# Optimization experiments

Hardware: AMD Instinct MI355X
Metric: run time of the kernel (lower is better)

The kernel has to match this reference:

```python
import jax, jax.numpy as jnp
import numpy as np

NUM_VARS = 50
EDGE_TYPES = 4
N_HID = 256
MSG_HID = N_HID // 8  # 32
IN_SIZE = 16
BATCH = 512
SKIP_FIRST = True

_adj = np.ones((NUM_VARS, NUM_VARS)) - np.eye(NUM_VARS)
SEND_EDGES, RECV_EDGES = np.where(_adj)
NUM_EDGES = SEND_EDGES.shape[0]  # 2450


def _lin(key, fan_in, fan_out):
    k1, k2 = jax.random.split(key)
    bound = 1.0 / np.sqrt(fan_in)
    w = jax.random.uniform(k1, (fan_in, fan_out), jnp.float32, -bound, bound)
    b = jax.random.uniform(k2, (fan_out,), jnp.float32, -bound, bound)
    return w, b


def setup_inputs() -> dict:
    key = jax.random.key(0)
    ks = jax.random.split(key, 10)
    inputs = jax.random.normal(ks[0], (BATCH, NUM_VARS, IN_SIZE), jnp.float32)
    edges = jax.random.uniform(ks[1], (BATCH, NUM_EDGES, EDGE_TYPES), jnp.float32)
    # per-edge-type message MLPs, stacked over edge-type axis
    f1 = [_lin(jax.random.fold_in(ks[2], i), 2 * IN_SIZE, MSG_HID) for i in range(EDGE_TYPES)]
    f2 = [_lin(jax.random.fold_in(ks[3], i), MSG_HID, MSG_HID) for i in range(EDGE_TYPES)]
    msg_fc1_w = jnp.stack([w for w, _ in f1]); msg_fc1_b = jnp.stack([b for _, b in f1])
    msg_fc2_w = jnp.stack([w for w, _ in f2]); msg_fc2_b = jnp.stack([b for _, b in f2])
    out_fc1_w, out_fc1_b = _lin(ks[4], IN_SIZE + MSG_HID, N_HID)
    out_fc2_w, out_fc2_b = _lin(ks[5], N_HID, N_HID)
    mu_w, mu_b = _lin(ks[6], N_HID, IN_SIZE)
    return dict(inputs=inputs, edges=edges,
                msg_fc1_w=msg_fc1_w, msg_fc1_b=msg_fc1_b,
                msg_fc2_w=msg_fc2_w, msg_fc2_b=msg_fc2_b,
                out_fc1_w=out_fc1_w, out_fc1_b=out_fc1_b,
                out_fc2_w=out_fc2_w, out_fc2_b=out_fc2_b,
                mu_w=mu_w, mu_b=mu_b)


def reference(inputs, edges, msg_fc1_w, msg_fc1_b, msg_fc2_w, msg_fc2_b,
              out_fc1_w, out_fc1_b, out_fc2_w, out_fc2_b, mu_w, mu_b):
    send = jnp.asarray(SEND_EDGES)
    recv = jnp.asarray(RECV_EDGES)
    # gather endpoints: [B, E, 2*in]
    pre_msg = jnp.concatenate([inputs[:, recv, :], inputs[:, send, :]], axis=-1)
    B = inputs.shape[0]
    all_msgs = jnp.zeros((B, NUM_EDGES, MSG_HID), inputs.dtype)
    start = 1 if SKIP_FIRST else 0
    for k in range(start, EDGE_TYPES):  # small fixed loop over edge types
        m = jax.nn.relu(pre_msg @ msg_fc1_w[k] + msg_fc1_b[k])
        m = jax.nn.relu(m @ msg_fc2_w[k] + msg_fc2_b[k])
        all_msgs = all_msgs + m * edges[:, :, k:k + 1]
    # scatter-sum edges -> receiver nodes (replaces dense edge2node_mat matmul)
    agg = jax.ops.segment_sum(jnp.swapaxes(all_msgs, 0, 1), recv,
                              num_segments=NUM_VARS)  # [V, B, H]
    agg = jnp.swapaxes(agg, 0, 1)  # [B, V, H]
    aug = jnp.concatenate([inputs, agg], axis=-1)
    pred = jax.nn.relu(aug @ out_fc1_w + out_fc1_b)
    pred = jax.nn.relu(pred @ out_fc2_w + out_fc2_b)
    mu = pred @ mu_w + mu_b  # eval mode: pi_action = mu (no rsample, dropout p=0)
    return (mu, pred)
```

## Files before the change

### kernel.cpp

```cpp
#include <hip/hip_runtime.h>
#include <hip/hip_bf16.h>

#define BATCHN 512
#define NV 50
#define NE 2450
#define INSZ 16
#define MH 32
#define NH 256

typedef short s16x8 __attribute__((ext_vector_type(8)));
typedef float f32x4 __attribute__((ext_vector_type(4)));
typedef float f32x2 __attribute__((ext_vector_type(2)));

#define PRED_OFF (BATCHN * NV * INSZ)


__device__ __forceinline__ unsigned short f2bf(float x) {
  unsigned int u = __float_as_uint(x);
  unsigned int r = (u + 0x7fffu + ((u >> 16) & 1u)) >> 16;
  return (unsigned short)r;
}
__device__ __forceinline__ unsigned int pk2(float a, float b) {
  return (unsigned int)f2bf(a) | ((unsigned int)f2bf(b) << 16);
}
__device__ __forceinline__ unsigned int cvtpk(float lo, float hi) {
  unsigned int r;
  asm("v_cvt_pk_bf16_f32 %0, %1, %2" : "=v"(r) : "v"(lo), "v"(hi));
  return r;
}
__device__ __forceinline__ unsigned int pkmax0(unsigned int x, unsigned int z) {
  unsigned int r;
  asm("v_pk_max_i16 %0, %1, %2" : "=v"(r) : "v"(x), "v"(z));
  return r;
}

__global__ void k_tr(const float* __restrict__ w1, const float* __restrict__ w2,
                     const float* __restrict__ wo1, const float* __restrict__ wo2,
                     const float* __restrict__ wmu,
                     unsigned short* __restrict__ W2t, unsigned short* __restrict__ W1t,
                     unsigned short* __restrict__ Wt1sw, unsigned short* __restrict__ Wt2sw,
                     unsigned short* __restrict__ Wtmusw) {
  int idx = blockIdx.x * 256 + threadIdx.x;
  if (idx < 3072) {
    int c = idx & 31, h = (idx >> 5) & 31, kk = idx >> 10;
    W2t[idx] = f2bf(w2[((kk + 1) * 32 + c) * 32 + h]);
  } else if (idx < 9216) {
    int j = idx - 3072;
    int k = j & 31, n = (j >> 5) & 31, kk = (j >> 10) % 3, half = j / 3072;
    W1t[j] = f2bf(k < 16 ? w1[((kk + 1) * 32 + half * 16 + k) * 32 + n] : 0.f);
  } else if (idx < 9216 + 16384) {
    int j = idx - 9216; int n = j & 255, kl = j >> 8;
    float v = kl < 48 ? wo1[kl * 256 + n] : 0.f;
    Wt1sw[n * 64 + (kl ^ ((n & 7) << 3))] = f2bf(v);
  } else if (idx < 9216 + 16384 + 65536) {
    int j = idx - (9216 + 16384);
    int c = j >> 14, r = j & 16383;
    int n = r & 255, kl = r >> 8;
    float v = wo2[(c * 64 + kl) * 256 + n];
    Wt2sw[(c * 256 + n) * 64 + (kl ^ ((n & 7) << 3))] = f2bf(v);
  } else if (idx < 9216 + 16384 + 65536 + 4096) {
    int j = idx - (9216 + 16384 + 65536);
    int n = j & 15, kl = j >> 4;
    Wtmusw[n * 256 + (kl ^ ((n & 7) << 3))] = f2bf(wmu[kl * 16 + n]);
  }
}

__global__ void __launch_bounds__(512, 4)
k_msg(const float* __restrict__ inputs, const float* __restrict__ edges,
      const float* __restrict__ b1, const float* __restrict__ b2,
      const unsigned short* __restrict__ W1t, const unsigned short* __restrict__ W2t,
      float* __restrict__ agg) {
  __shared__ __align__(16) float S_lds[NV * 100];
  __shared__ __align__(16) float R_lds[NV * 100];
  __shared__ __align__(16) float E_lds[NV * 156];

  const int b   = blockIdx.x;
  const int tid = threadIdx.x;
  const int w   = tid >> 6;
  const int l   = tid & 63;
  const int grp = l >> 4;
  const int lm  = l & 15;
  const int jt  = w & 3;
  const int ih  = w >> 2;

  for (int x = tid; x < NV * 52; x += 512) {
    int i  = x / 52;
    int js = x - i * 52;
    float4 ev = make_float4(0.f, 0.f, 0.f, 0.f);
    if (js < NV && js != i) {
      int e = i * 49 + js - (js > i ? 1 : 0);
      ev = reinterpret_cast<const float4*>(edges)[b * NE + e];
    }
    int base = i * 156 + js;
    E_lds[base]       = ev.y;
    E_lds[base + 52]  = ev.z;
    E_lds[base + 104] = ev.w;
  }

  {
    const int half = w >> 2;
    const int mt4  = w & 3;
    int node  = mt4 * 16 + lm;
    int nodec = node < NV ? node : NV - 1;
    s16x8 af = {0, 0, 0, 0, 0, 0, 0, 0};
    if (grp < 2) {
      const float4* ip = reinterpret_cast<const float4*>(inputs) + (b * NV + nodec) * 4 + grp * 2;
      float4 x0 = ip[0], x1 = ip[1];
      union { unsigned int u[4]; s16x8 v; } U;
      U.u[0] = cvtpk(x0.x, x0.y); U.u[1] = cvtpk(x0.z, x0.w);
      U.u[2] = cvtpk(x1.x, x1.y); U.u[3] = cvtpk(x1.z, x1.w);
      af = U.v;
    }
    float* dst = half ? S_lds : R_lds;
#pragma unroll
    for (int kk = 0; kk < 3; ++kk) {
#pragma unroll
      for (int nt = 0; nt < 2; ++nt) {
        int h = lm + 16 * nt;
        s16x8 bf = *reinterpret_cast<const s16x8*>(W1t + ((half * 3 + kk) * 32 + h) * 32 + grp * 8);
        f32x4 C;
        if (half == 0) { float bv = b1[(kk + 1) * 32 + h]; C = f32x4{bv, bv, bv, bv}; }
        else C = f32x4{0.f, 0.f, 0.f, 0.f};
        f32x4 o = __builtin_amdgcn_mfma_f32_16x16x32_bf16(af, bf, C, 0, 0, 0);
#pragma unroll
        for (int rr = 0; rr < 4; ++rr) {
          int n2 = mt4 * 16 + grp * 4 + rr;
          if (n2 < NV) dst[n2 * 100 + kk * 32 + h] = o[rr];
        }
      }
    }
  }

  s16x8 Bf[3][2];
  f32x4 Cb[3][2];
#pragma unroll
  for (int kk = 0; kk < 3; ++kk)
#pragma unroll
    for (int nt = 0; nt < 2; ++nt) {
      int h = lm + 16 * nt;
      Bf[kk][nt] = *reinterpret_cast<const s16x8*>(W2t + (kk * 32 + h) * 32 + grp * 8);
      float bv = b2[(kk + 1) * 32 + h];
      Cb[kk][nt] = f32x4{bv, bv, bv, bv};
    }
  const unsigned int zero = 0;
  __syncthreads();

  float Rreg[3][8];
  {
    int jrow = jt * 16 + lm;
    int jr   = jrow < NV ? jrow : NV - 1;
#pragma unroll
    for (int kk = 0; kk < 3; ++kk) {
      const float* Rp = &R_lds[jr * 100 + kk * 32 + grp * 8];
      f32x4 rA = *reinterpret_cast<const f32x4*>(Rp);
      f32x4 rB = *reinterpret_cast<const f32x4*>(Rp + 4);
#pragma unroll
      for (int p = 0; p < 4; ++p) { Rreg[kk][p] = rA[p]; Rreg[kk][4 + p] = rB[p]; }
    }
  }
  __syncthreads();

  const int slot0 = jt * 16 + grp * 4;
  const bool dead = slot0 > 48;
  const int slot  = dead ? 48 : slot0;

  f32x4 acc0 = {0.f, 0.f, 0.f, 0.f};
  f32x4 acc1 = {0.f, 0.f, 0.f, 0.f};

  for (int i = ih; i < NV; i += 2) {
    const float* Eb = &E_lds[i * 156 + slot];
#pragma unroll
    for (int kk = 0; kk < 3; ++kk) {
      const float* Sp = &S_lds[i * 100 + kk * 32 + grp * 8];
      f32x4 sA = *reinterpret_cast<const f32x4*>(Sp);
      f32x4 sB = *reinterpret_cast<const f32x4*>(Sp + 4);
      union { unsigned int u[4]; s16x8 v; } U;
      U.u[0] = pkmax0(cvtpk(Rreg[kk][0] + sA[0], Rreg[kk][1] + sA[1]), zero);
      U.u[1] = pkmax0(cvtpk(Rreg[kk][2] + sA[2], Rreg[kk][3] + sA[3]), zero);
      U.u[2] = pkmax0(cvtpk(Rreg[kk][4] + sB[0], Rreg[kk][5] + sB[1]), zero);
      U.u[3] = pkmax0(cvtpk(Rreg[kk][6] + sB[2], Rreg[kk][7] + sB[3]), zero);
      f32x4 d0 = __builtin_amdgcn_mfma_f32_16x16x32_bf16(U.v, Bf[kk][0], Cb[kk][0], 0, 0, 0);
      f32x4 d1 = __builtin_amdgcn_mfma_f32_16x16x32_bf16(U.v, Bf[kk][1], Cb[kk][1], 0, 0, 0);
      f32x4 ev = *reinterpret_cast<const f32x4*>(Eb + kk * 52);
      if (dead) ev = f32x4{0.f, 0.f, 0.f, 0.f};
#pragma unroll
      for (int rr = 0; rr < 4; ++rr) {
        acc0[rr] = fmaf(fmaxf(d0[rr], 0.f), ev[rr], acc0[rr]);
        acc1[rr] = fmaf(fmaxf(d1[rr], 0.f), ev[rr], acc1[rr]);
      }
    }
  }

  float* comb = R_lds;
  if (ih == 1) {
    int cbase = (jt * 64 + l) * 10;
    *reinterpret_cast<f32x2*>(&comb[cbase])     = f32x2{acc0[0], acc0[1]};
    *reinterpret_cast<f32x2*>(&comb[cbase + 2]) = f32x2{acc0[2], acc0[3]};
    *reinterpret_cast<f32x2*>(&comb[cbase + 4]) = f32x2{acc1[0], acc1[1]};
    *reinterpret_cast<f32x2*>(&comb[cbase + 6]) = f32x2{acc1[2], acc1[3]};
  }
  __syncthreads();
  if (ih == 0) {
    int cbase = (jt * 64 + l) * 10;
    f32x2 c0 = *reinterpret_cast<const f32x2*>(&comb[cbase]);
    f32x2 c1 = *reinterpret_cast<const f32x2*>(&comb[cbase + 2]);
    f32x2 c2 = *reinterpret_cast<const f32x2*>(&comb[cbase + 4]);
    f32x2 c3 = *reinterpret_cast<const f32x2*>(&comb[cbase + 6]);
    acc0[0] += c0[0]; acc0[1] += c0[1]; acc0[2] += c1[0]; acc0[3] += c1[1];
    acc1[0] += c2[0]; acc1[1] += c2[1]; acc1[2] += c3[0]; acc1[3] += c3[1];
#pragma unroll
    for (int rr = 0; rr < 4; ++rr) {
      int j = jt * 16 + grp * 4 + rr;
      if (j < NV) {
        agg[(b * NV + j) * MH + lm]      = acc0[rr];
        agg[(b * NV + j) * MH + 16 + lm] = acc1[rr];
      }
    }
  }
}

__global__ void __launch_bounds__(256, 3)
k_out(const float* __restrict__ inputs, const float* __restrict__ agg,
      const unsigned short* __restrict__ Wt1sw, const float* __restrict__ bo1,
      const unsigned short* __restrict__ Wt2sw, const float* __restrict__ bo2,
      const unsigned short* __restrict__ Wtmusw, const float* __restrict__ bmu,
      float* __restrict__ out) {
  __shared__ unsigned short aug[64 * 72];
  __shared__ unsigned short P1[64 * 264];
  __shared__ __align__(16) unsigned short WB[16384];

  const int tid = threadIdx.x;
  const int w   = tid >> 6;
  const int l   = tid & 63;
  const int grp = l >> 4;
  const int lm  = l & 15;
  const int gr0 = blockIdx.x * 64;
  const int xo  = (lm & 7) << 3;

  {
    int row = tid >> 2, q = tid & 3;
    int gr = gr0 + row;
    float4 iv = reinterpret_cast<const float4*>(inputs)[gr * 4 + q];
    uint2 u0; u0.x = pk2(iv.x, iv.y); u0.y = pk2(iv.z, iv.w);
    *reinterpret_cast<uint2*>(&aug[row * 72 + q * 4]) = u0;
    float4 a0 = reinterpret_cast<const float4*>(agg)[gr * 8 + q * 2];
    float4 a1 = reinterpret_cast<const float4*>(agg)[gr * 8 + q * 2 + 1];
    uint4 u1; u1.x = pk2(a0.x, a0.y); u1.y = pk2(a0.z, a0.w);
    u1.z = pk2(a1.x, a1.y); u1.w = pk2(a1.z, a1.w);
    *reinterpret_cast<uint4*>(&aug[row * 72 + 16 + q * 8]) = u1;
    uint2 uz; uz.x = 0u; uz.y = 0u;
    *reinterpret_cast<uint2*>(&aug[row * 72 + 48 + q * 4]) = uz;
  }
  {
    const uint4* src = reinterpret_cast<const uint4*>(Wt1sw);
    for (int i = tid; i < 2048; i += 256) reinterpret_cast<uint4*>(WB)[i] = src[i];
  }
  __syncthreads();

  const int rowA  = 16 * w + lm;
  const int kgrp  = grp * 8;
  const int rbase = 16 * w + grp * 4;

  f32x4 acc1[16];
#pragma unroll
  for (int nt = 0; nt < 16; ++nt) acc1[nt] = f32x4{0.f, 0.f, 0.f, 0.f};
#pragma unroll
  for (int kc = 0; kc < 2; ++kc) {
    s16x8 af = *reinterpret_cast<const s16x8*>(&aug[rowA * 72 + kc * 32 + kgrp]);
#pragma unroll
    for (int nt = 0; nt < 16; ++nt) {
      int n = lm + 16 * nt;
      s16x8 bf = *reinterpret_cast<const s16x8*>(&WB[n * 64 + ((kc * 32 + kgrp) ^ xo)]);
      acc1[nt] = __builtin_amdgcn_mfma_f32_16x16x32_bf16(af, bf, acc1[nt], 0, 0, 0);
    }
  }
#pragma unroll
  for (int nt = 0; nt < 16; ++nt) {
    int n = lm + 16 * nt;
    float bias = bo1[n];
#pragma unroll
    for (int rr = 0; rr < 4; ++rr) {
      float v = acc1[nt][rr] + bias; v = v > 0.f ? v : 0.f;
      P1[(rbase + rr) * 264 + n] = f2bf(v);
    }
  }
  __syncthreads();

  f32x4 acc2[16];
#pragma unroll
  for (int nt = 0; nt < 16; ++nt) acc2[nt] = f32x4{0.f, 0.f, 0.f, 0.f};
  for (int c = 0; c < 4; ++c) {
    const uint4* src = reinterpret_cast<const uint4*>(Wt2sw + c * 16384);
    for (int i = tid; i < 2048; i += 256) reinterpret_cast<uint4*>(WB)[i] = src[i];
    __syncthreads();
#pragma unroll
    for (int kcl = 0; kcl < 2; ++kcl) {
      int kc = c * 2 + kcl;
      s16x8 af = *reinterpret_cast<const s16x8*>(&P1[rowA * 264 + kc * 32 + kgrp]);
#pragma unroll
      for (int nt = 0; nt < 16; ++nt) {
        int n = lm + 16 * nt;
        s16x8 bf = *reinterpret_cast<const s16x8*>(&WB[n * 64 + ((kcl * 32 + kgrp) ^ xo)]);
        acc2[nt] = __builtin_amdgcn_mfma_f32_16x16x32_bf16(af, bf, acc2[nt], 0, 0, 0);
      }
    }
    __syncthreads();
  }
#pragma unroll
  for (int nt = 0; nt < 16; ++nt) {
    int n = lm + 16 * nt;
    float bias = bo2[n];
#pragma unroll
    for (int rr = 0; rr < 4; ++rr) {
      float v = acc2[nt][rr] + bias; v = v > 0.f ? v : 0.f;
      out[PRED_OFF + (gr0 + rbase + rr) * 256 + n] = v;
      P1[(rbase + rr) * 264 + n] = f2bf(v);
    }
  }

  {
    const uint4* src = reinterpret_cast<const uint4*>(Wtmusw);
    for (int i = tid; i < 512; i += 256) reinterpret_cast<uint4*>(WB)[i] = src[i];
  }
  __syncthreads();
  f32x4 accm = {0.f, 0.f, 0.f, 0.f};
#pragma unroll
  for (int kc = 0; kc < 8; ++kc) {
    s16x8 af = *reinterpret_cast<const s16x8*>(&P1[rowA * 264 + kc * 32 + kgrp]);
    s16x8 bf = *reinterpret_cast<const s16x8*>(&WB[lm * 256 + ((kc * 32 + kgrp) ^ xo)]);
    accm = __builtin_amdgcn_mfma_f32_16x16x32_bf16(af, bf, accm, 0, 0, 0);
  }
  {
    float bias = bmu[lm];
#pragma unroll
    for (int rr = 0; rr < 4; ++rr) {
      out[(gr0 + rbase + rr) * 16 + lm] = accm[rr] + bias;
    }
  }
}

extern "C" void kernel_launch(void* const* d_in, const int* in_sizes, int n_in,
                              void* d_out, int out_size, void* d_ws, size_t ws_size,
                              hipStream_t stream) {
  const float* inputs = (const float*)d_in[0];
  const float* edges  = (const float*)d_in[1];
  const float* w1     = (const float*)d_in[2];
  const float* b1     = (const float*)d_in[3];
  const float* w2     = (const float*)d_in[4];
  const float* b2     = (const float*)d_in[5];
  const float* wo1    = (const float*)d_in[6];
  const float* bo1    = (const float*)d_in[7];
  const float* wo2    = (const float*)d_in[8];
  const float* bo2    = (const float*)d_in[9];
  const float* wmu    = (const float*)d_in[10];
  const float* bmu    = (const float*)d_in[11];
  float* out = (float*)d_out;

  char* ws = (char*)d_ws;
  float*          agg    = (float*)(ws + 0);
  unsigned short* W2t    = (unsigned short*)(ws + 3276800);
  unsigned short* W1t    = (unsigned short*)(ws + 3282944);
  unsigned short* Wt1sw  = (unsigned short*)(ws + 3295232);
  unsigned short* Wt2sw  = (unsigned short*)(ws + 3328000);
  unsigned short* Wtmusw = (unsigned short*)(ws + 3459072);

  k_tr<<<372, 256, 0, stream>>>(w1, w2, wo1, wo2, wmu, W2t, W1t, Wt1sw, Wt2sw, Wtmusw);
  k_msg<<<512, 512, 0, stream>>>(inputs, edges, b1, b2, W1t, W2t, agg);
  k_out<<<400, 256, 0, stream>>>(inputs, agg, Wt1sw, bo1, Wt2sw, bo2, Wtmusw, bmu, out);
}
```

Measured before the change: 59.59 us.

## Fuse message and output MLP kernels into one per-batch kernel

Merges the message-passing kernel and the output MLP kernel into a single kernel per batch element. The aggregated messages stay in shared memory instead of going through a global workspace. Shared memory is reused across phases via one aliased buffer, and the output MLP work is split across the 8 warps by halving the N tiles per warp. The inner message loop also switches to packed f32 add/fma instructions and unrolls by 2. The risks are that 64-row tiles now pad 50 valid rows, so some MFMA work is wasted, and the larger LDS footprint may reduce occupancy.

```diff
diff --git a/kernel.cpp b/kernel.cpp
--- a/kernel.cpp
+++ b/kernel.cpp
@@ -32,6 +32,14 @@
   unsigned int r;
   asm("v_pk_max_i16 %0, %1, %2" : "=v"(r) : "v"(x), "v"(z));
   return r;
+}
+__device__ __forceinline__ f32x2 pkadd(f32x2 a, f32x2 b) {
+  f32x2 r;
+  asm("v_pk_add_f32 %0, %1, %2" : "=v"(r) : "v"(a), "v"(b));
+  return r;
+}
+__device__ __forceinline__ void pkfma(f32x2& acc, f32x2 a, f32x2 b) {
+  asm("v_pk_fma_f32 %0, %1, %2, %0" : "+v"(acc) : "v"(a), "v"(b));
 }
 
 __global__ void k_tr(const float* __restrict__ w1, const float* __restrict__ w2,
@@ -66,13 +74,22 @@
 }
 
 __global__ void __launch_bounds__(512, 4)
-k_msg(const float* __restrict__ inputs, const float* __restrict__ edges,
+k_all(const float* __restrict__ inputs, const float* __restrict__ edges,
       const float* __restrict__ b1, const float* __restrict__ b2,
       const unsigned short* __restrict__ W1t, const unsigned short* __restrict__ W2t,
-      float* __restrict__ agg) {
-  __shared__ __align__(16) float S_lds[NV * 100];
-  __shared__ __align__(16) float R_lds[NV * 100];
-  __shared__ __align__(16) float E_lds[NV * 156];
+      const unsigned short* __restrict__ Wt1sw, const float* __restrict__ bo1,
+      const unsigned short* __restrict__ Wt2sw, const float* __restrict__ bo2,
+      const unsigned short* __restrict__ Wtmusw, const float* __restrict__ bmu,
+      float* __restrict__ out) {
+  __shared__ __align__(16) char smem[75776];
+  float* S_lds = (float*)(smem);
+  float* R_lds = (float*)(smem + 20000);
+  float* E_lds = (float*)(smem + 40000);
+  float* comb  = (float*)(smem + 20000);
+  float* agg_l = (float*)(smem + 9216);
+  unsigned short* aug = (unsigned short*)(smem);
+  unsigned short* P1  = (unsigned short*)(smem + 9216);
+  unsigned short* WB  = (unsigned short*)(smem + 43008);
 
   const int b   = blockIdx.x;
   const int tid = threadIdx.x;
@@ -145,7 +162,7 @@
   const unsigned int zero = 0;
   __syncthreads();
 
-  float Rreg[3][8];
+  f32x2 Rp2[3][4];
   {
     int jrow = jt * 16 + lm;
     int jr   = jrow < NV ? jrow : NV - 1;
@@ -154,8 +171,8 @@
       const float* Rp = &R_lds[jr * 100 + kk * 32 + grp * 8];
       f32x4 rA = *reinterpret_cast<const f32x4*>(Rp);
       f32x4 rB = *reinterpret_cast<const f32x4*>(Rp + 4);
-#pragma unroll
-      for (int p = 0; p < 4; ++p) { Rreg[kk][p] = rA[p]; Rreg[kk][4 + p] = rB[p]; }
+      Rp2[kk][0] = f32x2{rA[0], rA[1]}; Rp2[kk][1] = f32x2{rA[2], rA[3]};
+      Rp2[kk][2] = f32x2{rB[0], rB[1]}; Rp2[kk][3] = f32x2{rB[2], rB[3]};
     }
   }
   __syncthreads();
@@ -164,9 +181,10 @@
   const bool dead = slot0 > 48;
   const int slot  = dead ? 48 : slot0;
 
-  f32x4 acc0 = {0.f, 0.f, 0.f, 0.f};
-  f32x4 acc1 = {0.f, 0.f, 0.f, 0.f};
-
+  f32x2 acc0a = {0.f, 0.f}, acc0b = {0.f, 0.f};
+  f32x2 acc1a = {0.f, 0.f}, acc1b = {0.f, 0.f};
+
+#pragma unroll 2
   for (int i = ih; i < NV; i += 2) {
     const float* Eb = &E_lds[i * 156 + slot];
 #pragma unroll
@@ -174,109 +192,101 @@
       const float* Sp = &S_lds[i * 100 + kk * 32 + grp * 8];
       f32x4 sA = *reinterpret_cast<const f32x4*>(Sp);
       f32x4 sB = *reinterpret_cast<const f32x4*>(Sp + 4);
+      f32x2 t0 = pkadd(Rp2[kk][0], f32x2{sA[0], sA[1]});
+      f32x2 t1 = pkadd(Rp2[kk][1], f32x2{sA[2], sA[3]});
+      f32x2 t2 = pkadd(Rp2[kk][2], f32x2{sB[0], sB[1]});
+      f32x2 t3 = pkadd(Rp2[kk][3], f32x2{sB[2], sB[3]});
       union { unsigned int u[4]; s16x8 v; } U;
-      U.u[0] = pkmax0(cvtpk(Rreg[kk][0] + sA[0], Rreg[kk][1] + sA[1]), zero);
-      U.u[1] = pkmax0(cvtpk(Rreg[kk][2] + sA[2], Rreg[kk][3] + sA[3]), zero);
-      U.u[2] = pkmax0(cvtpk(Rreg[kk][4] + sB[0], Rreg[kk][5] + sB[1]), zero);
-      U.u[3] = pkmax0(cvtpk(Rreg[kk][6] + sB[2], Rreg[kk][7] + sB[3]), zero);
+      U.u[0] = pkmax0(cvtpk(t0[0], t0[1]), zero);
+      U.u[1] = pkmax0(cvtpk(t1[0], t1[1]), zero);
+      U.u[2] = pkmax0(cvtpk(t2[0], t2[1]), zero);
+      U.u[3] = pkmax0(cvtpk(t3[0], t3[1]), zero);
       f32x4 d0 = __builtin_amdgcn_mfma_f32_16x16x32_bf16(U.v, Bf[kk][0], Cb[kk][0], 0, 0, 0);
       f32x4 d1 = __builtin_amdgcn_mfma_f32_16x16x32_bf16(U.v, Bf[kk][1], Cb[kk][1], 0, 0, 0);
       f32x4 ev = *reinterpret_cast<const f32x4*>(Eb + kk * 52);
       if (dead) ev = f32x4{0.f, 0.f, 0.f, 0.f};
-#pragma unroll
-      for (int rr = 0; rr < 4; ++rr) {
-        acc0[rr] = fmaf(fmaxf(d0[rr], 0.f), ev[rr], acc0[rr]);
-        acc1[rr] = fmaf(fmaxf(d1[rr], 0.f), ev[rr], acc1[rr]);
-      }
-    }
-  }
-
-  float* comb = R_lds;
+      f32x2 ea = {ev[0], ev[1]}, eb = {ev[2], ev[3]};
+      f32x2 r0a = {fmaxf(d0[0], 0.f), fmaxf(d0[1], 0.f)};
+      f32x2 r0b = {fmaxf(d0[2], 0.f), fmaxf(d0[3], 0.f)};
+      f32x2 r1a = {fmaxf(d1[0], 0.f), fmaxf(d1[1], 0.f)};
+      f32x2 r1b = {fmaxf(d1[2], 0.f), fmaxf(d1[3], 0.f)};
+      pkfma(acc0a, r0a, ea); pkfma(acc0b, r0b, eb);
+      pkfma(acc1a, r1a, ea); pkfma(acc1b, r1b, eb);
+    }
+  }
+
   if (ih == 1) {
     int cbase = (jt * 64 + l) * 10;
-    *reinterpret_cast<f32x2*>(&comb[cbase])     = f32x2{acc0[0], acc0[1]};
-    *reinterpret_cast<f32x2*>(&comb[cbase + 2]) = f32x2{acc0[2], acc0[3]};
-    *reinterpret_cast<f32x2*>(&comb[cbase + 4]) = f32x2{acc1[0], acc1[1]};
-    *reinterpret_cast<f32x2*>(&comb[cbase + 6]) = f32x2{acc1[2], acc1[3]};
+    *reinterpret_cast<f32x2*>(&comb[cbase])     = acc0a;
+    *reinterpret_cast<f32x2*>(&comb[cbase + 2]) = acc0b;
+    *reinterpret_cast<f32x2*>(&comb[cbase + 4]) = acc1a;
+    *reinterpret_cast<f32x2*>(&comb[cbase + 6]) = acc1b;
   }
   __syncthreads();
   if (ih == 0) {
     int cbase = (jt * 64 + l) * 10;
-    f32x2 c0 = *reinterpret_cast<const f32x2*>(&comb[cbase]);
-    f32x2 c1 = *reinterpret_cast<const f32x2*>(&comb[cbase + 2]);
-    f32x2 c2 = *reinterpret_cast<const f32x2*>(&comb[cbase + 4]);
-    f32x2 c3 = *reinterpret_cast<const f32x2*>(&comb[cbase + 6]);
-    acc0[0] += c0[0]; acc0[1] += c0[1]; acc0[2] += c1[0]; acc0[3] += c1[1];
-    acc1[0] += c2[0]; acc1[1] += c2[1]; acc1[2] += c3[0]; acc1[3] += c3[1];
+    acc0a += *reinterpret_cast<const f32x2*>(&comb[cbase]);
+    acc0b += *reinterpret_cast<const f32x2*>(&comb[cbase + 2]);
+    acc1a += *reinterpret_cast<const f32x2*>(&comb[cbase + 4]);
+    acc1b += *reinterpret_cast<const f32x2*>(&comb[cbase + 6]);
+    float a0v[4] = {acc0a[0], acc0a[1], acc0b[0], acc0b[1]};
+    float a1v[4] = {acc1a[0], acc1a[1], acc1b[0], acc1b[1]};
 #pragma unroll
     for (int rr = 0; rr < 4; ++rr) {
       int j = jt * 16 + grp * 4 + rr;
       if (j < NV) {
-        agg[(b * NV + j) * MH + lm]      = acc0[rr];
-        agg[(b * NV + j) * MH + 16 + lm] = acc1[rr];
+        agg_l[j * 32 + lm]      = a0v[rr];
+        agg_l[j * 32 + 16 + lm] = a1v[rr];
       }
     }
   }
-}
-
-__global__ void __launch_bounds__(256, 3)
-k_out(const float* __restrict__ inputs, const float* __restrict__ agg,
-      const unsigned short* __restrict__ Wt1sw, const float* __restrict__ bo1,
-      const unsigned short* __restrict__ Wt2sw, const float* __restrict__ bo2,
-      const unsigned short* __restrict__ Wtmusw, const float* __restrict__ bmu,
-      float* __restrict__ out) {
-  __shared__ unsigned short aug[64 * 72];
-  __shared__ unsigned short P1[64 * 264];
-  __shared__ __align__(16) unsigned short WB[16384];
-
-  const int tid = threadIdx.x;
-  const int w   = tid >> 6;
-  const int l   = tid & 63;
-  const int grp = l >> 4;
-  const int lm  = l & 15;
-  const int gr0 = blockIdx.x * 64;
-  const int xo  = (lm & 7) << 3;
-
-  {
+  __syncthreads();
+
+  const int xo = (lm & 7) << 3;
+
+  if (tid < 256) {
     int row = tid >> 2, q = tid & 3;
-    int gr = gr0 + row;
-    float4 iv = reinterpret_cast<const float4*>(inputs)[gr * 4 + q];
-    uint2 u0; u0.x = pk2(iv.x, iv.y); u0.y = pk2(iv.z, iv.w);
+    uint2 u0; uint4 u1;
+    if (row < NV) {
+      float4 iv = reinterpret_cast<const float4*>(inputs)[(b * NV + row) * 4 + q];
+      u0.x = pk2(iv.x, iv.y); u0.y = pk2(iv.z, iv.w);
+      f32x4 a0 = *reinterpret_cast<const f32x4*>(&agg_l[row * 32 + q * 8]);
+      f32x4 a1 = *reinterpret_cast<const f32x4*>(&agg_l[row * 32 + q * 8 + 4]);
+      u1.x = pk2(a0[0], a0[1]); u1.y = pk2(a0[2], a0[3]);
+      u1.z = pk2(a1[0], a1[1]); u1.w = pk2(a1[2], a1[3]);
+    } else { u0.x = u0.y = 0u; u1.x = u1.y = u1.z = u1.w = 0u; }
     *reinterpret_cast<uint2*>(&aug[row * 72 + q * 4]) = u0;
-    float4 a0 = reinterpret_cast<const float4*>(agg)[gr * 8 + q * 2];
-    float4 a1 = reinterpret_cast<const float4*>(agg)[gr * 8 + q * 2 + 1];
-    uint4 u1; u1.x = pk2(a0.x, a0.y); u1.y = pk2(a0.z, a0.w);
-    u1.z = pk2(a1.x, a1.y); u1.w = pk2(a1.z, a1.w);
     *reinterpret_cast<uint4*>(&aug[row * 72 + 16 + q * 8]) = u1;
     uint2 uz; uz.x = 0u; uz.y = 0u;
     *reinterpret_cast<uint2*>(&aug[row * 72 + 48 + q * 4]) = uz;
   }
   {
     const uint4* src = reinterpret_cast<const uint4*>(Wt1sw);
-    for (int i = tid; i < 2048; i += 256) reinterpret_cast<uint4*>(WB)[i] = src[i];
-  }
-  __syncthreads();
-
-  const int rowA  = 16 * w + lm;
+    for (int i2 = tid; i2 < 2048; i2 += 512) reinterpret_cast<uint4*>(WB)[i2] = src[i2];
+  }
+  __syncthreads();
+
+  const int rowA  = 16 * jt + lm;
   const int kgrp  = grp * 8;
-  const int rbase = 16 * w + grp * 4;
-
-  f32x4 acc1[16];
-#pragma unroll
-  for (int nt = 0; nt < 16; ++nt) acc1[nt] = f32x4{0.f, 0.f, 0.f, 0.f};
+  const int rbase = 16 * jt + grp * 4;
+  const int n0    = ih * 8;
+
+  f32x4 acc1[8];
+#pragma unroll
+  for (int nt = 0; nt < 8; ++nt) acc1[nt] = f32x4{0.f, 0.f, 0.f, 0.f};
 #pragma unroll
   for (int kc = 0; kc < 2; ++kc) {
     s16x8 af = *reinterpret_cast<const s16x8*>(&aug[rowA * 72 + kc * 32 + kgrp]);
 #pragma unroll
-    for (int nt = 0; nt < 16; ++nt) {
-      int n = lm + 16 * nt;
+    for (int nt = 0; nt < 8; ++nt) {
+      int n = lm + 16 * (n0 + nt);
       s16x8 bf = *reinterpret_cast<const s16x8*>(&WB[n * 64 + ((kc * 32 + kgrp) ^ xo)]);
       acc1[nt] = __builtin_amdgcn_mfma_f32_16x16x32_bf16(af, bf, acc1[nt], 0, 0, 0);
     }
   }
 #pragma unroll
-  for (int nt = 0; nt < 16; ++nt) {
-    int n = lm + 16 * nt;
+  for (int nt = 0; nt < 8; ++nt) {
+    int n = lm + 16 * (n0 + nt);
     float bias = bo1[n];
 #pragma unroll
     for (int rr = 0; rr < 4; ++rr) {
@@ -286,20 +296,20 @@
   }
   __syncthreads();
 
-  f32x4 acc2[16];
-#pragma unroll
-  for (int nt = 0; nt < 16; ++nt) acc2[nt] = f32x4{0.f, 0.f, 0.f, 0.f};
+  f32x4 acc2[8];
+#pragma unroll
+  for (int nt = 0; nt < 8; ++nt) acc2[nt] = f32x4{0.f, 0.f, 0.f, 0.f};
   for (int c = 0; c < 4; ++c) {
     const uint4* src = reinterpret_cast<const uint4*>(Wt2sw + c * 16384);
-    for (int i = tid; i < 2048; i += 256) reinterpret_cast<uint4*>(WB)[i] = src[i];
+    for (int i2 = tid; i2 < 2048; i2 += 512) reinterpret_cast<uint4*>(WB)[i2] = src[i2];
     __syncthreads();
 #pragma unroll
     for (int kcl = 0; kcl < 2; ++kcl) {
       int kc = c * 2 + kcl;
       s16x8 af = *reinterpret_cast<const s16x8*>(&P1[rowA * 264 + kc * 32 + kgrp]);
 #pragma unroll
-      for (int nt = 0; nt < 16; ++nt) {
-        int n = lm + 16 * nt;
+      for (int nt = 0; nt < 8; ++nt) {
+        int n = lm + 16 * (n0 + nt);
         s16x8 bf = *reinterpret_cast<const s16x8*>(&WB[n * 64 + ((kcl * 32 + kgrp) ^ xo)]);
         acc2[nt] = __builtin_amdgcn_mfma_f32_16x16x32_bf16(af, bf, acc2[nt], 0, 0, 0);
       }
@@ -307,34 +317,33 @@
     __syncthreads();
   }
 #pragma unroll
-  for (int nt = 0; nt < 16; ++nt) {
-    int n = lm + 16 * nt;
+  for (int nt = 0; nt < 8; ++nt) {
+    int n = lm + 16 * (n0 + nt);
     float bias = bo2[n];
 #pragma unroll
     for (int rr = 0; rr < 4; ++rr) {
+      int row = rbase + rr;
       float v = acc2[nt][rr] + bias; v = v > 0.f ? v : 0.f;
-      out[PRED_OFF + (gr0 + rbase + rr) * 256 + n] = v;
-      P1[(rbase + rr) * 264 + n] = f2bf(v);
-    }
-  }
-
-  {
-    const uint4* src = reinterpret_cast<const uint4*>(Wtmusw);
-    for (int i = tid; i < 512; i += 256) reinterpret_cast<uint4*>(WB)[i] = src[i];
-  }
-  __syncthreads();
-  f32x4 accm = {0.f, 0.f, 0.f, 0.f};
-#pragma unroll
-  for (int kc = 0; kc < 8; ++kc) {
-    s16x8 af = *reinterpret_cast<const s16x8*>(&P1[rowA * 264 + kc * 32 + kgrp]);
-    s16x8 bf = *reinterpret_cast<const s16x8*>(&WB[lm * 256 + ((kc * 32 + kgrp) ^ xo)]);
-    accm = __builtin_amdgcn_mfma_f32_16x16x32_bf16(af, bf, accm, 0, 0, 0);
-  }
-  {
+      if (row < NV) out[PRED_OFF + (b * NV + row) * 256 + n] = v;
+      P1[row * 264 + n] = f2bf(v);
+    }
+  }
+  reinterpret_cast<uint4*>(WB)[tid] = reinterpret_cast<const uint4*>(Wtmusw)[tid];
+  __syncthreads();
+
+  if (ih == 0) {
+    f32x4 accm = {0.f, 0.f, 0.f, 0.f};
+#pragma unroll
+    for (int kc = 0; kc < 8; ++kc) {
+      s16x8 af = *reinterpret_cast<const s16x8*>(&P1[rowA * 264 + kc * 32 + kgrp]);
+      s16x8 bf = *reinterpret_cast<const s16x8*>(&WB[lm * 256 + ((kc * 32 + kgrp) ^ xo)]);
+      accm = __builtin_amdgcn_mfma_f32_16x16x32_bf16(af, bf, accm, 0, 0, 0);
+    }
     float bias = bmu[lm];
 #pragma unroll
     for (int rr = 0; rr < 4; ++rr) {
-      out[(gr0 + rbase + rr) * 16 + lm] = accm[rr] + bias;
+      int row = rbase + rr;
+      if (row < NV) out[(b * NV + row) * 16 + lm] = accm[rr] + bias;
     }
   }
 }
@@ -357,7 +366,6 @@
   float* out = (float*)d_out;
 
   char* ws = (char*)d_ws;
-  float*          agg    = (float*)(ws + 0);
   unsigned short* W2t    = (unsigned short*)(ws + 3276800);
   unsigned short* W1t    = (unsigned short*)(ws + 3282944);
   unsigned short* Wt1sw  = (unsigned short*)(ws + 3295232);
@@ -365,6 +373,6 @@
   unsigned short* Wtmusw = (unsigned short*)(ws + 3459072);
 
   k_tr<<<372, 256, 0, stream>>>(w1, w2, wo1, wo2, wmu, W2t, W1t, Wt1sw, Wt2sw, Wtmusw);
-  k_msg<<<512, 512, 0, stream>>>(inputs, edges, b1, b2, W1t, W2t, agg);
-  k_out<<<400, 256, 0, stream>>>(inputs, agg, Wt1sw, bo1, Wt2sw, bo2, Wtmusw, bmu, out);
-}
+  k_all<<<512, 512, 0, stream>>>(inputs, edges, b1, b2, W1t, W2t,
+                                 Wt1sw, bo1, Wt2sw, bo2, Wtmusw, bmu, out);
+}
```

New measurement: 55.11 us. -7.5%, faster.
